# Optimization experiments

Measured on AMD Instinct MI355X. Metric: run time of the kernel, lower is better.

## Reference

```python
import jax, jax.numpy as jnp
import numpy as np
from jax import lax

D = 2048; H = 32; N = 64; S = 2048
LW = 64; LA = 64; LG = 128; LV = 32


def _ln(z, w, b, eps):
    m = jnp.mean(z, axis=-1, keepdims=True)
    v = jnp.var(z, axis=-1, keepdims=True)
    return (z - m) * lax.rsqrt(v + eps) * w + b


def setup_inputs():
    ks = iter(jax.random.split(jax.random.key(0), 40))
    nrm = lambda shape, s=1.0: jax.random.normal(next(ks), shape, dtype=jnp.float32) * s
    return {
        "x": nrm((1, S, D)),
        "state1": nrm((D,)),
        "state2": nrm((H, N, N), 0.1),
        "v_first": nrm((S, H, N)),
        "ln1_w": jnp.ones((D,), jnp.float32),
        "ln1_b": jnp.zeros((D,), jnp.float32),
        "x_r": nrm((D,), 0.1), "x_w": nrm((D,), 0.1), "x_k": nrm((D,), 0.1),
        "x_v": nrm((D,), 0.1), "x_a": nrm((D,), 0.1), "x_g": nrm((D,), 0.1),
        "Wr": nrm((D, D), 0.02), "Wk": nrm((D, D), 0.02),
        "Wv": nrm((D, D), 0.02), "Wo": nrm((D, D), 0.02),
        "w1": nrm((D, LW), 0.02), "w2": nrm((LW, D), 0.05), "w0": nrm((D,), 0.1),
        "a1": nrm((D, LA), 0.02), "a2": nrm((LA, D), 0.05), "a0": nrm((D,), 0.1),
        "g1": nrm((D, LG), 0.02), "g2": nrm((LG, D), 0.05),
        "v1": nrm((D, LV), 0.02), "v2": nrm((LV, D), 0.05), "v0": nrm((D,), 0.1),
        "k_k": nrm((H, N), 0.5), "k_a": nrm((H, N), 0.5), "r_k": nrm((H, N), 0.5),
        "ln_x_w": jnp.ones((D,), jnp.float32),
        "ln_x_b": jnp.zeros((D,), jnp.float32),
    }


def _forward(x, state1, state2, v_first, ln1_w, ln1_b, x_r, x_w, x_k, x_v, x_a, x_g,
             Wr, Wk, Wv, Wo, w1, w2, w0, a1, a2, a0, g1, g2, v1, v2, v0,
             k_k, k_a, r_k, ln_x_w, ln_x_b):
    last_x = x
    xn = _ln(x, ln1_w, ln1_b, 1e-5)                      # (1,S,D)
    state1_out = xn[:, -1:]
    past = jnp.concatenate([state1.reshape(1, 1, D), xn[:, :-1]], axis=1)
    sx = past - xn                                        # token-shift delta
    xr = xn + sx * x_r; xw = xn + sx * x_w; xk = xn + sx * x_k
    xv = xn + sx * x_v; xa = xn + sx * x_a; xg = xn + sx * x_g
    r = (xr @ Wr.T).reshape(S, H, N)
    k = (xk @ Wk.T).reshape(S, H, N)
    v = (xv @ Wv.T).reshape(S, H, N)
    gate = jax.nn.sigmoid(xg @ g1) @ g2                   # (1,S,D)
    a = jax.nn.sigmoid((xa @ a1) @ a2 + a0).reshape(S, H, N)
    td = jnp.tanh(xw @ w1) @ w2 + w0
    w_dec = jnp.exp(-0.606531 * jax.nn.sigmoid(td)).reshape(S, H, N)
    kk = k * k_k
    kk = kk / jnp.maximum(jnp.linalg.norm(kk, axis=-1, keepdims=True), 1e-12)
    k = k * (1.0 + (a - 1.0) * k_a)
    # layer_id != 0: residual value mixing with v_first
    v = v + (v_first - v) * jax.nn.sigmoid(((xv @ v1) @ v2 + v0).reshape(S, H, N))
    b = kk * a
    a_neg = -kk

    def step(s, inp):
        # s: (H,N,N) state; each input (H,N)
        r_t, w_t, k_t, v_t, a_t, b_t = inp
        sa = jnp.einsum('hij,hj->hi', s, a_t)
        s = s * w_t[:, None, :] + sa[:, :, None] * b_t[:, None, :] + v_t[:, :, None] * k_t[:, None, :]
        return s, jnp.einsum('hij,hj->hi', s, r_t)

    state2_out, y = lax.scan(step, state2, (r, w_dec, k, v, a_neg, b))  # y: (S,H,N)
    o = _ln(y, 1.0, 0.0, 0.00064).reshape(1, S, D)       # ln_x (default affine)
    o = o * ln_x_w + ln_x_b
    rkv = (jnp.sum(r * k * r_k, axis=-1, keepdims=True) * v).reshape(1, S, D)
    o = (o + rkv) * gate
    o = o @ Wo.T
    return last_x + o, state1_out, state2_out


def reference(x, state1, state2, v_first, ln1_w, ln1_b, x_r, x_w, x_k, x_v, x_a, x_g,
              Wr, Wk, Wv, Wo, w1, w2, w0, a1, a2, a0, g1, g2, v1, v2, v0,
              k_k, k_a, r_k, ln_x_w, ln_x_b):
    return _forward(x, state1, state2, v_first, ln1_w, ln1_b, x_r, x_w, x_k, x_v, x_a, x_g,
                    Wr, Wk, Wv, Wo, w1, w2, w0, a1, a2, a0, g1, g2, v1, v2, v0,
                    k_k, k_a, r_k, ln_x_w, ln_x_b)
```

## Files before the change

kernel.cpp:

```cpp
#include <hip/hip_runtime.h>
#include <math.h>

#define kD 2048
#define kH 32
#define kN 64
#define kS 2048

typedef unsigned short ushort_t;
typedef unsigned int uint32;

__device__ __forceinline__ ushort_t f2bf(float f) {
  uint32 u = __float_as_uint(f);
  u += 0x7fffu + ((u >> 16) & 1u);
  return (ushort_t)(u >> 16);
}
__device__ __forceinline__ float bf2f(ushort_t u) {
  return __uint_as_float(((uint32)u) << 16);
}
__device__ __forceinline__ float sigm(float x) { return 1.f / (1.f + __expf(-x)); }

__global__ __launch_bounds__(256) void ln1_kernel(
    const float* __restrict__ x, const float* __restrict__ w, const float* __restrict__ b,
    ushort_t* __restrict__ xnbf, ushort_t* __restrict__ xprevbf,
    const float* __restrict__ state1, float* __restrict__ state1_out)
{
  int t = blockIdx.x;
  const float* row = x + (size_t)t * kD;
  float s = 0.f, s2 = 0.f;
  for (int d = threadIdx.x; d < kD; d += 256) {
    float v = row[d]; s += v; s2 += v * v;
  }
  #pragma unroll
  for (int o = 32; o > 0; o >>= 1) { s += __shfl_down(s, o); s2 += __shfl_down(s2, o); }
  __shared__ float ls[4], ls2[4];
  int wid = threadIdx.x >> 6;
  if ((threadIdx.x & 63) == 0) { ls[wid] = s; ls2[wid] = s2; }
  __syncthreads();
  s = ls[0] + ls[1] + ls[2] + ls[3];
  s2 = ls2[0] + ls2[1] + ls2[2] + ls2[3];
  float mean = s * (1.f / kD);
  float var = s2 * (1.f / kD) - mean * mean;
  float rstd = rsqrtf(var + 1e-5f);
  for (int d = threadIdx.x; d < kD; d += 256) {
    float v = (row[d] - mean) * rstd * w[d] + b[d];
    ushort_t bf = f2bf(v);
    xnbf[(size_t)t * kD + d] = bf;
    if (t < kS - 1) xprevbf[(size_t)(t + 1) * kD + d] = bf;
    else state1_out[d] = v;
    if (t == 0) xprevbf[d] = f2bf(state1[d]);
  }
}

__global__ __launch_bounds__(256) void mix3_cvt(
    const ushort_t* __restrict__ xnbf, const ushort_t* __restrict__ xprevbf,
    const float* __restrict__ cr, const float* __restrict__ ck, const float* __restrict__ cv,
    ushort_t* __restrict__ Ar, ushort_t* __restrict__ Ak, ushort_t* __restrict__ Av)
{
  int t = blockIdx.x;
  size_t base = (size_t)t * kD;
  for (int d = threadIdx.x; d < kD; d += 256) {
    float c = bf2f(xnbf[base + d]);
    float dx = bf2f(xprevbf[base + d]) - c;
    Ar[base + d] = f2bf(c + dx * cr[d]);
    Ak[base + d] = f2bf(c + dx * ck[d]);
    Av[base + d] = f2bf(c + dx * cv[d]);
  }
}

struct CvtArgs { const float* src[3]; ushort_t* dst[3]; };
__global__ __launch_bounds__(256) void cvt_bf16_b(CvtArgs args)
{
  const float* in = args.src[blockIdx.y];
  ushort_t* out = args.dst[blockIdx.y];
  int idx = blockIdx.x * 256 + threadIdx.x;
  float4 v = ((const float4*)in)[idx];
  ushort_t o[4] = { f2bf(v.x), f2bf(v.y), f2bf(v.z), f2bf(v.w) };
  ((uint2*)out)[idx] = *(const uint2*)o;
}

typedef __bf16 bf16x8 __attribute__((ext_vector_type(8)));
typedef float f32x4 __attribute__((ext_vector_type(4)));

struct GemmArgs {
  const ushort_t* A[3];
  const ushort_t* B[3];
  float* C[3];
  const float* resid[3];
};

__global__ __launch_bounds__(256) void gemm_bf16_b(GemmArgs args)
{
  int z = blockIdx.z;
  const ushort_t* __restrict__ A = args.A[z];
  const ushort_t* __restrict__ B = args.B[z];
  float* __restrict__ C = args.C[z];
  const float* __restrict__ resid = args.resid[z];

  __shared__ __align__(16) ushort_t As[128 * 64];
  __shared__ __align__(16) ushort_t Bs[128 * 64];
  int tid = threadIdx.x;
  int w = tid >> 6, lane = tid & 63;
  int row0 = blockIdx.y * 128, col0 = blockIdx.x * 128;
  int wrow = (w >> 1) * 64, wcol = (w & 1) * 64;
  int quad = lane >> 4, r16 = lane & 15;
  f32x4 acc[4][4] = {};

  int lrow = lane >> 3;
  int lsw  = (lane & 7) ^ lrow;

  for (int k0 = 0; k0 < kD; k0 += 64) {
    #pragma unroll
    for (int n = 0; n < 4; n++) {
      int rr = w * 32 + n * 8 + lrow;
      int cc = k0 + lsw * 8;
      const ushort_t* ga = A + (size_t)(row0 + rr) * kD + cc;
      const ushort_t* gb = B + (size_t)(col0 + rr) * kD + cc;
      __builtin_amdgcn_global_load_lds(
          (const __attribute__((address_space(1))) uint32*)ga,
          (__attribute__((address_space(3))) uint32*)&As[(w * 32 + n * 8) * 64], 16, 0, 0);
      __builtin_amdgcn_global_load_lds(
          (const __attribute__((address_space(1))) uint32*)gb,
          (__attribute__((address_space(3))) uint32*)&Bs[(w * 32 + n * 8) * 64], 16, 0, 0);
    }
    __syncthreads();
    #pragma unroll
    for (int kk = 0; kk < 64; kk += 32) {
      bf16x8 af[4], bfr[4];
      #pragma unroll
      for (int i = 0; i < 4; i++) {
        int row = wrow + i * 16 + r16;
        int chunk = ((kk >> 3) + quad) ^ (r16 & 7);
        af[i] = *(const bf16x8*)&As[row * 64 + chunk * 8];
      }
      #pragma unroll
      for (int j = 0; j < 4; j++) {
        int row = wcol + j * 16 + r16;
        int chunk = ((kk >> 3) + quad) ^ (r16 & 7);
        bfr[j] = *(const bf16x8*)&Bs[row * 64 + chunk * 8];
      }
      #pragma unroll
      for (int i = 0; i < 4; i++)
        #pragma unroll
        for (int j = 0; j < 4; j++)
          acc[i][j] = __builtin_amdgcn_mfma_f32_16x16x32_bf16(af[i], bfr[j], acc[i][j], 0, 0, 0);
    }
    __syncthreads();
  }
  #pragma unroll
  for (int i = 0; i < 4; i++) {
    #pragma unroll
    for (int j = 0; j < 4; j++) {
      int col = col0 + wcol + j * 16 + r16;
      #pragma unroll
      for (int reg = 0; reg < 4; reg++) {
        int row = row0 + wrow + i * 16 + quad * 4 + reg;
        float v = acc[i][j][reg];
        if (resid) v += resid[(size_t)row * kD + col];
        C[(size_t)row * kD + col] = v;
      }
    }
  }
}

struct PrepW1Args { const float* w1[4]; const float* c[4]; ushort_t* B1; };
__global__ __launch_bounds__(256) void prep_w1(PrepW1Args a)
{
  __shared__ float tile[64][17];
  int k0 = blockIdx.x * 64;
  int col0 = blockIdx.y * 16;
  int z, lc0, L;
  if (col0 < 128)      { z = 0; lc0 = col0;       L = 128; }
  else if (col0 < 192) { z = 1; lc0 = col0 - 128; L = 64; }
  else if (col0 < 256) { z = 2; lc0 = col0 - 192; L = 64; }
  else if (col0 < 288) { z = 3; lc0 = col0 - 256; L = 32; }
  else z = -1;
  int tid = threadIdx.x;
  if (z >= 0) {
    const float* W = a.w1[z];
    const float* C = a.c[z];
    int cc = tid & 15, kk = tid >> 4;
    #pragma unroll
    for (int i = 0; i < 4; i++) {
      int k = k0 + kk + i * 16;
      int ksrc = k & (kD - 1);
      float cv = C[ksrc];
      float sc = (k < kD) ? (1.f - cv) : cv;
      tile[kk + i * 16][cc] = W[(size_t)ksrc * L + lc0 + cc] * sc;
    }
  }
  __syncthreads();
  int kk2 = tid & 63, cc2 = tid >> 6;
  #pragma unroll
  for (int i = 0; i < 4; i++) {
    int col = col0 + cc2 * 4 + i;
    float v = (z >= 0) ? tile[kk2][cc2 * 4 + i] : 0.f;
    a.B1[(size_t)col * 4096 + k0 + kk2] = f2bf(v);
  }
}

struct PrepW2Args { const float* w2[4]; ushort_t* B2[4]; int L[4]; };
__global__ __launch_bounds__(256) void prep_w2(PrepW2Args a)
{
  __shared__ float tile[64][17];
  int z = blockIdx.z;
  int L = a.L[z];
  int l0 = blockIdx.y * 16;
  if (l0 >= L) return;
  int j0 = blockIdx.x * 64;
  int tid = threadIdx.x;
  const float* W = a.w2[z];
  ushort_t* out = a.B2[z];
  int jj = tid & 63;
  #pragma unroll
  for (int i = 0; i < 4; i++) {
    int ll = (tid >> 6) * 4 + i;
    tile[jj][ll] = W[(size_t)(l0 + ll) * kD + j0 + jj];
  }
  __syncthreads();
  int ll2 = tid & 15;
  #pragma unroll
  for (int i = 0; i < 4; i++) {
    int jj2 = (tid >> 4) + i * 16;
    out[(size_t)(j0 + jj2) * L + l0 + ll2] = f2bf(tile[jj2][ll2]);
  }
}

__global__ __launch_bounds__(256) void gemm1_kernel(
    const ushort_t* __restrict__ xnbf, const ushort_t* __restrict__ xprevbf,
    const ushort_t* __restrict__ B1, ushort_t* __restrict__ H)
{
  __shared__ __align__(16) ushort_t As[128 * 64];
  __shared__ __align__(16) ushort_t Bs[64 * 64];
  int tid = threadIdx.x;
  int w = tid >> 6, lane = tid & 63;
  int col0 = blockIdx.x * 64, row0 = blockIdx.y * 128;
  int quad = lane >> 4, r16 = lane & 15;
  f32x4 acc[2][4] = {};
  int lrow = lane >> 3;
  int lsw = (lane & 7) ^ lrow;

  for (int k0 = 0; k0 < 4096; k0 += 64) {
    const ushort_t* Abase = (k0 < kD) ? (xnbf + k0) : (xprevbf + (k0 - kD));
    #pragma unroll
    for (int n = 0; n < 4; n++) {
      int rr = w * 32 + n * 8 + lrow;
      const ushort_t* ga = Abase + (size_t)(row0 + rr) * kD + lsw * 8;
      __builtin_amdgcn_global_load_lds(
          (const __attribute__((address_space(1))) uint32*)ga,
          (__attribute__((address_space(3))) uint32*)&As[(w * 32 + n * 8) * 64], 16, 0, 0);
    }
    #pragma unroll
    for (int n = 0; n < 2; n++) {
      int rr = w * 16 + n * 8 + lrow;
      const ushort_t* gb = B1 + (size_t)(col0 + rr) * 4096 + k0 + lsw * 8;
      __builtin_amdgcn_global_load_lds(
          (const __attribute__((address_space(1))) uint32*)gb,
          (__attribute__((address_space(3))) uint32*)&Bs[(w * 16 + n * 8) * 64], 16, 0, 0);
    }
    __syncthreads();
    #pragma unroll
    for (int kk = 0; kk < 64; kk += 32) {
      bf16x8 af[2], bfr[4];
      #pragma unroll
      for (int i = 0; i < 2; i++) {
        int row = w * 32 + i * 16 + r16;
        int chunk = ((kk >> 3) + quad) ^ (r16 & 7);
        af[i] = *(const bf16x8*)&As[row * 64 + chunk * 8];
      }
      #pragma unroll
      for (int j = 0; j < 4; j++) {
        int row = j * 16 + r16;
        int chunk = ((kk >> 3) + quad) ^ (r16 & 7);
        bfr[j] = *(const bf16x8*)&Bs[row * 64 + chunk * 8];
      }
      #pragma unroll
      for (int i = 0; i < 2; i++)
        #pragma unroll
        for (int j = 0; j < 4; j++)
          acc[i][j] = __builtin_amdgcn_mfma_f32_16x16x32_bf16(af[i], bfr[j], acc[i][j], 0, 0, 0);
    }
    __syncthreads();
  }
  #pragma unroll
  for (int i = 0; i < 2; i++) {
    #pragma unroll
    for (int j = 0; j < 4; j++) {
      int col = col0 + j * 16 + r16;
      #pragma unroll
      for (int reg = 0; reg < 4; reg++) {
        int row = row0 + w * 32 + i * 16 + quad * 4 + reg;
        float v = acc[i][j][reg];
        if (col < 128) v = sigm(v);
        else if (col >= 192 && col < 256) v = tanhf(v);
        H[(size_t)row * 320 + col] = f2bf(v);
      }
    }
  }
}

struct Gemm2Args {
  const ushort_t* H;
  const ushort_t* B2[4];
  int Aofs[4];
  int L[4];
  const float* bias[4];
  float* out[4];
  const float* vfirst;
};
__global__ __launch_bounds__(256) void gemm2_kernel(Gemm2Args a)
{
  int z = blockIdx.z;
  int L = a.L[z];
  int nch = L >> 3;
  int rs = __builtin_ctz(nch);
  int mask = (nch >= 8) ? 7 : (nch - 1);
  __shared__ __align__(16) ushort_t As[128 * 128];
  __shared__ __align__(16) ushort_t Bs[128 * 128];
  int tid = threadIdx.x;
  int w = tid >> 6, lane = tid & 63;
  int row0 = blockIdx.y * 128, col0 = blockIdx.x * 128;
  int wrow = (w >> 1) * 64, wcol = (w & 1) * 64;
  int quad = lane >> 4, r16 = lane & 15;
  const ushort_t* A = a.H + a.Aofs[z];
  const ushort_t* B = a.B2[z];

  int nld = (128 * nch) >> 8;
  for (int i = 0; i < nld; i++) {
    int c = i * 256 + w * 64 + lane;
    int row = c >> rs;
    int ch = c & (nch - 1);
    int gch = ch ^ (row & mask);
    __builtin_amdgcn_global_load_lds(
        (const __attribute__((address_space(1))) uint32*)(A + (size_t)(row0 + row) * 320 + gch * 8),
        (__attribute__((address_space(3))) uint32*)&As[(i * 256 + w * 64) * 8], 16, 0, 0);
    __builtin_amdgcn_global_load_lds(
        (const __attribute__((address_space(1))) uint32*)(B + (size_t)(col0 + row) * L + gch * 8),
        (__attribute__((address_space(3))) uint32*)&Bs[(i * 256 + w * 64) * 8], 16, 0, 0);
  }
  __syncthreads();

  f32x4 acc[4][4] = {};
  int ksteps = L >> 5;
  for (int ks = 0; ks < ksteps; ks++) {
    bf16x8 af[4], bfr[4];
    #pragma unroll
    for (int i = 0; i < 4; i++) {
      int row = wrow + i * 16 + r16;
      int slot = ((ks << 2) + quad) ^ (r16 & mask);
      af[i] = *(const bf16x8*)&As[row * L + slot * 8];
    }
    #pragma unroll
    for (int j = 0; j < 4; j++) {
      int row = wcol + j * 16 + r16;
      int slot = ((ks << 2) + quad) ^ (r16 & mask);
      bfr[j] = *(const bf16x8*)&Bs[row * L + slot * 8];
    }
    #pragma unroll
    for (int i = 0; i < 4; i++)
      #pragma unroll
      for (int j = 0; j < 4; j++)
        acc[i][j] = __builtin_amdgcn_mfma_f32_16x16x32_bf16(af[i], bfr[j], acc[i][j], 0, 0, 0);
  }

  const float* bias = a.bias[z];
  float* C = a.out[z];
  #pragma unroll
  for (int i = 0; i < 4; i++) {
    #pragma unroll
    for (int j = 0; j < 4; j++) {
      int col = col0 + wcol + j * 16 + r16;
      #pragma unroll
      for (int reg = 0; reg < 4; reg++) {
        int row = row0 + wrow + i * 16 + quad * 4 + reg;
        float s = acc[i][j][reg];
        size_t idx = (size_t)row * kD + col;
        if (z == 0) {
          C[idx] = s;
        } else if (z == 1) {
          C[idx] = sigm(s + bias[col]);
        } else if (z == 2) {
          C[idx] = __expf(-0.606531f * sigm(s + bias[col]));
        } else {
          float vv = C[idx];
          C[idx] = vv + (a.vfirst[idx] - vv) * sigm(s + bias[col]);
        }
      }
    }
  }
}

__global__ __launch_bounds__(256) void post_kernel(
    float* __restrict__ kArr, float* __restrict__ kkArr, float* __restrict__ bArr,
    const float* __restrict__ aArr, float* __restrict__ rArr, const float* __restrict__ wArr,
    const float* __restrict__ k_k, const float* __restrict__ k_a, const float* __restrict__ r_k,
    float* __restrict__ c12, float* __restrict__ c3)
{
  int gid = blockIdx.x * 4 + (threadIdx.x >> 6);
  int lane = threadIdx.x & 63;
  int h = gid & (kH - 1);
  int d = h * kN + lane;
  size_t off = (size_t)gid * kN + lane;
  float kv = kArr[off];
  float kkv = kv * k_k[d];
  float ss = kkv * kkv;
  #pragma unroll
  for (int o = 32; o > 0; o >>= 1) ss += __shfl_xor(ss, o);
  float scale = 1.f / fmaxf(sqrtf(ss), 1e-12f);
  float kkf = kkv * scale;
  kkArr[off] = -kkf;
  float av = aArr[off];
  float bv = kkf * av;
  bArr[off] = bv;
  float knew = kv * (1.f + (av - 1.f) * k_a[d]);
  kArr[off] = knew;
  float rv = rArr[off];
  float wv = wArr[off];
  rArr[off] = wv * rv;
  float p1 = bv * rv;
  float p2 = knew * rv;
  float p3 = rv * knew * r_k[d];
  #pragma unroll
  for (int o = 32; o > 0; o >>= 1) {
    p1 += __shfl_xor(p1, o); p2 += __shfl_xor(p2, o); p3 += __shfl_xor(p3, o);
  }
  if (lane == 0) {
    c12[(size_t)gid * 2]     = p1;
    c12[(size_t)gid * 2 + 1] = p2;
    c3[gid] = p3;
  }
}

#define SLOT_F 344
#define NSLOT 24

__device__ __forceinline__ void row_allsum2(float& x, float& y) {
  int t;
  t = __builtin_amdgcn_update_dpp(0, __float_as_int(x), 0x121, 0xF, 0xF, true);
  x += __int_as_float(t);
  t = __builtin_amdgcn_update_dpp(0, __float_as_int(y), 0x121, 0xF, 0xF, true);
  y += __int_as_float(t);
  t = __builtin_amdgcn_update_dpp(0, __float_as_int(x), 0x122, 0xF, 0xF, true);
  x += __int_as_float(t);
  t = __builtin_amdgcn_update_dpp(0, __float_as_int(y), 0x122, 0xF, 0xF, true);
  y += __int_as_float(t);
  t = __builtin_amdgcn_update_dpp(0, __float_as_int(x), 0x124, 0xF, 0xF, true);
  x += __int_as_float(t);
  t = __builtin_amdgcn_update_dpp(0, __float_as_int(y), 0x124, 0xF, 0xF, true);
  y += __int_as_float(t);
  t = __builtin_amdgcn_update_dpp(0, __float_as_int(x), 0x128, 0xF, 0xF, true);
  x += __int_as_float(t);
  t = __builtin_amdgcn_update_dpp(0, __float_as_int(y), 0x128, 0xF, 0xF, true);
  y += __int_as_float(t);
}

__global__ __launch_bounds__(320) void scan_kernel(
    const float* __restrict__ s0_in, const float* __restrict__ wA, const float* __restrict__ wrA,
    const float* __restrict__ kA, const float* __restrict__ vA, const float* __restrict__ kkA,
    const float* __restrict__ bA, const float* __restrict__ c12,
    float* __restrict__ y, float* __restrict__ s_out)
{
  __shared__ __align__(16) float ring[NSLOT * SLOT_F];
  int blk = blockIdx.x;
  int h = blk >> 2;
  int i0 = (blk & 3) << 4;
  int wid = threadIdx.x >> 6;
  int lane = threadIdx.x & 63;
  int hv = h * kN;

  if (wid == 0) {
    const float* src0 = wA + hv;
    const float* src1 = wrA + hv;
    const float* src2 = kA + hv;
    const float* src3 = kkA + hv;
    const float* src4 = bA + hv;
    const float* vsrc = vA + hv + i0;
    const float* csrc = c12 + (size_t)h * 2;
    int slot = 0;
    #define ISSUE(t)                                                                     \
      {                                                                                  \
        float* sb = &ring[slot * SLOT_F];                                                \
        size_t go = (size_t)(t) * kD + lane;                                             \
        __builtin_amdgcn_global_load_lds(                                                \
            (const __attribute__((address_space(1))) uint32*)(src0 + go),                \
            (__attribute__((address_space(3))) uint32*)(sb + 0), 4, 0, 0);               \
        __builtin_amdgcn_global_load_lds(                                                \
            (const __attribute__((address_space(1))) uint32*)(src1 + go),                \
            (__attribute__((address_space(3))) uint32*)(sb + 64), 4, 0, 0);              \
        __builtin_amdgcn_global_load_lds(                                                \
            (const __attribute__((address_space(1))) uint32*)(src2 + go),                \
            (__attribute__((address_space(3))) uint32*)(sb + 128), 4, 0, 0);             \
        __builtin_amdgcn_global_load_lds(                                                \
            (const __attribute__((address_space(1))) uint32*)(src3 + go),                \
            (__attribute__((address_space(3))) uint32*)(sb + 192), 4, 0, 0);             \
        __builtin_amdgcn_global_load_lds(                                                \
            (const __attribute__((address_space(1))) uint32*)(src4 + go),                \
            (__attribute__((address_space(3))) uint32*)(sb + 256), 4, 0, 0);             \
        if (lane < 16)                                                                   \
          __builtin_amdgcn_global_load_lds(                                              \
              (const __attribute__((address_space(1))) uint32*)(vsrc + (size_t)(t) * kD + lane), \
              (__attribute__((address_space(3))) uint32*)(sb + 320), 4, 0, 0);           \
        if (lane < 2)                                                                    \
          __builtin_amdgcn_global_load_lds(                                              \
              (const __attribute__((address_space(1))) uint32*)(csrc + (size_t)(t) * (kH * 2) + lane), \
              (__attribute__((address_space(3))) uint32*)(sb + 336), 4, 0, 0);           \
        slot++; if (slot == NSLOT) slot = 0;                                             \
      }
    for (int t = 0; t < 16; t++) ISSUE(t);
    __syncthreads();
    for (int ph = 0; ph < kS / 8; ph++) {
      int t0 = ph * 8 + 16;
      if (t0 < kS) {
        for (int s = 0; s < 8; s++) ISSUE(t0 + s);
      }
      __syncthreads();
    }
    #undef ISSUE
  } else {
    int col16 = lane & 15;
    int row = lane >> 4;
    int vidx = (wid - 1) * 4 + row;
    int i = i0 + vidx;
    int co = col16 * 4;
    size_t srow = ((size_t)(hv + i)) * kN + co;
    float4 sS = *(const float4*)(s0_in + srow);
    float* py = y + (size_t)(hv + i);

    __syncthreads();

    float4 Aw4, Awr4, Ak4, Akk4, Ab4; float Av1, Ac1, Ac2;
    float4 Bw4, Bwr4, Bk4, Bkk4, Bb4; float Bv1, Bc1, Bc2;

    #define LOADSLOT(sl, W, WR, K, KK, B, V, C1, C2)             \
      {                                                          \
        const float* sb = &ring[(sl) * SLOT_F];                  \
        W  = *(const float4*)(sb + co);                          \
        WR = *(const float4*)(sb + 64 + co);                     \
        K  = *(const float4*)(sb + 128 + co);                    \
        KK = *(const float4*)(sb + 192 + co);                    \
        B  = *(const float4*)(sb + 256 + co);                    \
        V  = sb[320 + vidx];                                     \
        C1 = sb[336];                                            \
        C2 = sb[337];                                            \
      }
    #define STEP(W, WR, K, KK, B, V, C1, C2)                                  \
      {                                                                       \
        float sa = sS.x * KK.x + sS.y * KK.y + sS.z * KK.z + sS.w * KK.w;     \
        float u  = sS.x * WR.x + sS.y * WR.y + sS.z * WR.z + sS.w * WR.w;     \
        row_allsum2(sa, u);                                                   \
        sS.x = fmaf(sS.x, W.x, fmaf(sa, B.x, V * K.x));                       \
        sS.y = fmaf(sS.y, W.y, fmaf(sa, B.y, V * K.y));                       \
        sS.z = fmaf(sS.z, W.z, fmaf(sa, B.z, V * K.z));                       \
        sS.w = fmaf(sS.w, W.w, fmaf(sa, B.w, V * K.w));                       \
        float yv = fmaf(sa, C1, fmaf(V, C2, u));                              \
        if (col16 == 0) *py = yv;                                             \
        py += kD;                                                             \
      }

    LOADSLOT(0, Aw4, Awr4, Ak4, Akk4, Ab4, Av1, Ac1, Ac2);
    int slot = 1;
    for (int ph = 0; ph < kS / 8; ph++) {
      #pragma unroll
      for (int s = 0; s < 8; s += 2) {
        LOADSLOT(slot, Bw4, Bwr4, Bk4, Bkk4, Bb4, Bv1, Bc1, Bc2);
        slot++; if (slot == NSLOT) slot = 0;
        STEP(Aw4, Awr4, Ak4, Akk4, Ab4, Av1, Ac1, Ac2);
        LOADSLOT(slot, Aw4, Awr4, Ak4, Akk4, Ab4, Av1, Ac1, Ac2);
        slot++; if (slot == NSLOT) slot = 0;
        STEP(Bw4, Bwr4, Bk4, Bkk4, Bb4, Bv1, Bc1, Bc2);
      }
      __syncthreads();
    }
    #undef LOADSLOT
    #undef STEP
    *(float4*)(s_out + srow) = sS;
  }
}

__global__ __launch_bounds__(256) void out_kernel(
    const float* __restrict__ y, const float* __restrict__ vA, const float* __restrict__ c3,
    const float* __restrict__ lnw, const float* __restrict__ lnb,
    const float* __restrict__ gate, ushort_t* __restrict__ Ay)
{
  int gid = blockIdx.x * 4 + (threadIdx.x >> 6);
  int lane = threadIdx.x & 63;
  int h = gid & (kH - 1);
  size_t off = (size_t)gid * kN + lane;
  float yv = y[off];
  float s = yv, s2 = yv * yv;
  #pragma unroll
  for (int o = 32; o > 0; o >>= 1) { s += __shfl_xor(s, o); s2 += __shfl_xor(s2, o); }
  float mean = s * (1.f / kN);
  float var = s2 * (1.f / kN) - mean * mean;
  float o1 = (yv - mean) * rsqrtf(var + 0.00064f);
  int d = h * kN + lane;
  float ov = o1 * lnw[d] + lnb[d];
  float rkv = c3[gid] * vA[off];
  Ay[off] = f2bf((ov + rkv) * gate[off]);
}

extern "C" void kernel_launch(void* const* d_in, const int* in_sizes, int n_in,
                              void* d_out, int out_size, void* d_ws, size_t ws_size,
                              hipStream_t stream)
{
  const float* x      = (const float*)d_in[0];
  const float* state1 = (const float*)d_in[1];
  const float* state2 = (const float*)d_in[2];
  const float* vfirst = (const float*)d_in[3];
  const float* ln1w   = (const float*)d_in[4];
  const float* ln1b   = (const float*)d_in[5];
  const float* xr_c   = (const float*)d_in[6];
  const float* xw_c   = (const float*)d_in[7];
  const float* xk_c   = (const float*)d_in[8];
  const float* xv_c   = (const float*)d_in[9];
  const float* xa_c   = (const float*)d_in[10];
  const float* xg_c   = (const float*)d_in[11];
  const float* Wr     = (const float*)d_in[12];
  const float* Wk     = (const float*)d_in[13];
  const float* Wv     = (const float*)d_in[14];
  const float* Wo     = (const float*)d_in[15];
  const float* w1     = (const float*)d_in[16];
  const float* w2     = (const float*)d_in[17];
  const float* w0     = (const float*)d_in[18];
  const float* a1     = (const float*)d_in[19];
  const float* a2     = (const float*)d_in[20];
  const float* a0     = (const float*)d_in[21];
  const float* g1     = (const float*)d_in[22];
  const float* g2     = (const float*)d_in[23];
  const float* v1     = (const float*)d_in[24];
  const float* v2     = (const float*)d_in[25];
  const float* v0     = (const float*)d_in[26];
  const float* k_k    = (const float*)d_in[27];
  const float* k_a    = (const float*)d_in[28];
  const float* r_k    = (const float*)d_in[29];
  const float* lnxw   = (const float*)d_in[30];
  const float* lnxb   = (const float*)d_in[31];

  float* out0  = (float*)d_out;
  float* s1out = out0 + (size_t)kS * kD;
  float* s2out = s1out + kD;

  size_t SD = (size_t)kS * kD;
  float* ws  = (float*)d_ws;
  float* xnB = ws;
  float* rB  = ws + SD;
  float* kB  = ws + 2 * SD;
  float* vB  = ws + 3 * SD;
  float* wB  = ws + 4 * SD;
  float* aB  = ws + 5 * SD;
  float* kkB = ws + 6 * SD;
  float* bB  = ws + 7 * SD;
  float* gB  = ws + 8 * SD;
  float* yB  = ws + 9 * SD;

  ushort_t* xnbf    = (ushort_t*)xnB;
  ushort_t* xprevbf = (ushort_t*)xnB + SD;
  ushort_t* ArB = (ushort_t*)kkB;
  ushort_t* AkB = (ushort_t*)kkB + SD;
  ushort_t* AvB = (ushort_t*)bB;
  ushort_t* B1  = (ushort_t*)bB + SD;
  ushort_t* Hbuf = B1 + (size_t)320 * 4096;
  ushort_t* B2g  = Hbuf + (size_t)2048 * 320;
  ushort_t* B2a  = B2g + (size_t)2048 * 128;
  ushort_t* B2w  = B2a + (size_t)2048 * 64;
  ushort_t* B2v  = B2w + (size_t)2048 * 64;
  ushort_t* WrB = (ushort_t*)yB;
  ushort_t* WkB = (ushort_t*)yB + SD;
  ushort_t* WvB = (ushort_t*)gB;
  ushort_t* AyB = (ushort_t*)aB;
  ushort_t* WoB = (ushort_t*)rB;
  float* c12B = xnB;
  float* c3B  = xnB + (size_t)kS * kH * 2;

  ln1_kernel<<<kS, 256, 0, stream>>>(x, ln1w, ln1b, xnbf, xprevbf, state1, s1out);
  mix3_cvt<<<kS, 256, 0, stream>>>(xnbf, xprevbf, xr_c, xk_c, xv_c, ArB, AkB, AvB);

  const int CVT_BLKS = (int)(SD / 4 / 256);
  {
    CvtArgs ca;
    ca.src[0] = Wr; ca.src[1] = Wk; ca.src[2] = Wv;
    ca.dst[0] = WrB; ca.dst[1] = WkB; ca.dst[2] = WvB;
    cvt_bf16_b<<<dim3(CVT_BLKS, 3), 256, 0, stream>>>(ca);
  }
  {
    PrepW1Args pa;
    pa.w1[0] = g1; pa.w1[1] = a1; pa.w1[2] = w1; pa.w1[3] = v1;
    pa.c[0] = xg_c; pa.c[1] = xa_c; pa.c[2] = xw_c; pa.c[3] = xv_c;
    pa.B1 = B1;
    prep_w1<<<dim3(64, 20), 256, 0, stream>>>(pa);
  }
  {
    PrepW2Args pa;
    pa.w2[0] = g2; pa.w2[1] = a2; pa.w2[2] = w2; pa.w2[3] = v2;
    pa.B2[0] = B2g; pa.B2[1] = B2a; pa.B2[2] = B2w; pa.B2[3] = B2v;
    pa.L[0] = 128; pa.L[1] = 64; pa.L[2] = 64; pa.L[3] = 32;
    prep_w2<<<dim3(32, 8, 4), 256, 0, stream>>>(pa);
  }
  {
    GemmArgs ga;
    ga.A[0] = ArB; ga.A[1] = AkB; ga.A[2] = AvB;
    ga.B[0] = WrB; ga.B[1] = WkB; ga.B[2] = WvB;
    ga.C[0] = rB;  ga.C[1] = kB;  ga.C[2] = vB;
    ga.resid[0] = nullptr; ga.resid[1] = nullptr; ga.resid[2] = nullptr;
    gemm_bf16_b<<<dim3(16, 16, 3), 256, 0, stream>>>(ga);
  }

  gemm1_kernel<<<dim3(5, 16), 256, 0, stream>>>(xnbf, xprevbf, B1, Hbuf);
  {
    Gemm2Args ga;
    ga.H = Hbuf;
    ga.B2[0] = B2g; ga.B2[1] = B2a; ga.B2[2] = B2w; ga.B2[3] = B2v;
    ga.Aofs[0] = 0; ga.Aofs[1] = 128; ga.Aofs[2] = 192; ga.Aofs[3] = 256;
    ga.L[0] = 128; ga.L[1] = 64; ga.L[2] = 64; ga.L[3] = 32;
    ga.bias[0] = nullptr; ga.bias[1] = a0; ga.bias[2] = w0; ga.bias[3] = v0;
    ga.out[0] = gB; ga.out[1] = aB; ga.out[2] = wB; ga.out[3] = vB;
    ga.vfirst = vfirst;
    gemm2_kernel<<<dim3(16, 16, 4), 256, 0, stream>>>(ga);
  }

  post_kernel<<<kS * kH / 4, 256, 0, stream>>>(kB, kkB, bB, aB, rB, wB,
                                               k_k, k_a, r_k, c12B, c3B);

  scan_kernel<<<kH * 4, 320, 0, stream>>>(state2, wB, rB, kB, vB, kkB, bB, c12B, yB, s2out);

  out_kernel<<<kS * kH / 4, 256, 0, stream>>>(yB, vB, c3B, lnxw, lnxb, gB, AyB);

  {
    CvtArgs ca;
    ca.src[0] = Wo; ca.src[1] = Wo; ca.src[2] = Wo;
    ca.dst[0] = WoB; ca.dst[1] = WoB; ca.dst[2] = WoB;
    cvt_bf16_b<<<dim3(CVT_BLKS, 1), 256, 0, stream>>>(ca);
  }
  {
    GemmArgs ga;
    ga.A[0] = AyB; ga.A[1] = AyB; ga.A[2] = AyB;
    ga.B[0] = WoB; ga.B[1] = WoB; ga.B[2] = WoB;
    ga.C[0] = out0; ga.C[1] = out0; ga.C[2] = out0;
    ga.resid[0] = x; ga.resid[1] = x; ga.resid[2] = x;
    gemm_bf16_b<<<dim3(16, 16, 1), 256, 0, stream>>>(ga);
  }
}
```

Measured before the change: 795.8 us.

## Use 16-byte global_load_lds in scan producer and widen ring phases

The scan kernel's producer wave now issues two 16-byte-per-lane global-to-LDS loads per timestep instead of seven 4-byte loads. Lanes are assigned to the w/wr/k/kk rows, the b row, the v slice and the padded c12 pair. c12 is padded to a stride of 4 floats so it stays 16-byte aligned. The ring grows to 32 slots with 16-step phases, which halves barrier frequency, and blocks are remapped so neighbouring blocks cover different heads. The aim is to cut per-step load-issue overhead and barrier syncs on the serial recurrence, at the cost of more LDS use.

```diff
diff --git a/kernel.cpp b/kernel.cpp
--- a/kernel.cpp
+++ b/kernel.cpp
@@ -424,14 +424,15 @@
     p1 += __shfl_xor(p1, o); p2 += __shfl_xor(p2, o); p3 += __shfl_xor(p3, o);
   }
   if (lane == 0) {
-    c12[(size_t)gid * 2]     = p1;
-    c12[(size_t)gid * 2 + 1] = p2;
+    c12[(size_t)gid * 4]     = p1;
+    c12[(size_t)gid * 4 + 1] = p2;
     c3[gid] = p3;
   }
 }
 
 #define SLOT_F 344
-#define NSLOT 24
+#define NSLOT 32
+#define PHASE 16
 
 __device__ __forceinline__ void row_allsum2(float& x, float& y) {
   int t;
@@ -461,56 +462,40 @@
 {
   __shared__ __align__(16) float ring[NSLOT * SLOT_F];
   int blk = blockIdx.x;
-  int h = blk >> 2;
-  int i0 = (blk & 3) << 4;
+  int h = blk & 31;
+  int i0 = (blk >> 5) << 4;
   int wid = threadIdx.x >> 6;
   int lane = threadIdx.x & 63;
   int hv = h * kN;
 
   if (wid == 0) {
-    const float* src0 = wA + hv;
-    const float* src1 = wrA + hv;
-    const float* src2 = kA + hv;
-    const float* src3 = kkA + hv;
-    const float* src4 = bA + hv;
-    const float* vsrc = vA + hv + i0;
-    const float* csrc = c12 + (size_t)h * 2;
-    int slot = 0;
-    #define ISSUE(t)                                                                     \
-      {                                                                                  \
-        float* sb = &ring[slot * SLOT_F];                                                \
-        size_t go = (size_t)(t) * kD + lane;                                             \
-        __builtin_amdgcn_global_load_lds(                                                \
-            (const __attribute__((address_space(1))) uint32*)(src0 + go),                \
-            (__attribute__((address_space(3))) uint32*)(sb + 0), 4, 0, 0);               \
-        __builtin_amdgcn_global_load_lds(                                                \
-            (const __attribute__((address_space(1))) uint32*)(src1 + go),                \
-            (__attribute__((address_space(3))) uint32*)(sb + 64), 4, 0, 0);              \
-        __builtin_amdgcn_global_load_lds(                                                \
-            (const __attribute__((address_space(1))) uint32*)(src2 + go),                \
-            (__attribute__((address_space(3))) uint32*)(sb + 128), 4, 0, 0);             \
-        __builtin_amdgcn_global_load_lds(                                                \
-            (const __attribute__((address_space(1))) uint32*)(src3 + go),                \
-            (__attribute__((address_space(3))) uint32*)(sb + 192), 4, 0, 0);             \
-        __builtin_amdgcn_global_load_lds(                                                \
-            (const __attribute__((address_space(1))) uint32*)(src4 + go),                \
-            (__attribute__((address_space(3))) uint32*)(sb + 256), 4, 0, 0);             \
-        if (lane < 16)                                                                   \
-          __builtin_amdgcn_global_load_lds(                                              \
-              (const __attribute__((address_space(1))) uint32*)(vsrc + (size_t)(t) * kD + lane), \
-              (__attribute__((address_space(3))) uint32*)(sb + 320), 4, 0, 0);           \
-        if (lane < 2)                                                                    \
-          __builtin_amdgcn_global_load_lds(                                              \
-              (const __attribute__((address_space(1))) uint32*)(csrc + (size_t)(t) * (kH * 2) + lane), \
-              (__attribute__((address_space(3))) uint32*)(sb + 336), 4, 0, 0);           \
-        slot++; if (slot == NSLOT) slot = 0;                                             \
-      }
-    for (int t = 0; t < 16; t++) ISSUE(t);
+    int sel = lane >> 4;
+    const float* b1 = (sel == 0) ? wA : (sel == 1) ? wrA : (sel == 2) ? kA : kkA;
+    b1 += hv + (lane & 15) * 4;
+    const float* b2;
+    size_t st2;
+    if (lane < 16)      { b2 = bA + hv + lane * 4;             st2 = kD; }
+    else if (lane < 20) { b2 = vA + hv + i0 + (lane - 16) * 4; st2 = kD; }
+    else                { b2 = c12 + (size_t)h * 4;            st2 = kH * 4; }
+    bool m2 = (lane < 21);
+
+    #define ISSUE(t)                                                                       \
+      {                                                                                    \
+        float* sb = &ring[((t) & (NSLOT - 1)) * SLOT_F];                                   \
+        __builtin_amdgcn_global_load_lds(                                                  \
+            (const __attribute__((address_space(1))) uint32*)(b1 + (size_t)(t) * kD),      \
+            (__attribute__((address_space(3))) uint32*)sb, 16, 0, 0);                      \
+        if (m2)                                                                            \
+          __builtin_amdgcn_global_load_lds(                                                \
+              (const __attribute__((address_space(1))) uint32*)(b2 + (size_t)(t) * st2),   \
+              (__attribute__((address_space(3))) uint32*)(sb + 256), 16, 0, 0);            \
+      }
+    for (int t = 0; t < PHASE; t++) ISSUE(t);
     __syncthreads();
-    for (int ph = 0; ph < kS / 8; ph++) {
-      int t0 = ph * 8 + 16;
+    for (int ph = 0; ph < kS / PHASE; ph++) {
+      int t0 = ph * PHASE + PHASE;
       if (t0 < kS) {
-        for (int s = 0; s < 8; s++) ISSUE(t0 + s);
+        for (int t = t0; t < t0 + PHASE; t++) ISSUE(t);
       }
       __syncthreads();
     }
@@ -556,16 +541,15 @@
         py += kD;                                                             \
       }
 
-    LOADSLOT(0, Aw4, Awr4, Ak4, Akk4, Ab4, Av1, Ac1, Ac2);
-    int slot = 1;
-    for (int ph = 0; ph < kS / 8; ph++) {
-      #pragma unroll
-      for (int s = 0; s < 8; s += 2) {
-        LOADSLOT(slot, Bw4, Bwr4, Bk4, Bkk4, Bb4, Bv1, Bc1, Bc2);
-        slot++; if (slot == NSLOT) slot = 0;
+    for (int ph = 0; ph < kS / PHASE; ph++) {
+      int t0 = ph * PHASE;
+      LOADSLOT(t0 & (NSLOT - 1), Aw4, Awr4, Ak4, Akk4, Ab4, Av1, Ac1, Ac2);
+      #pragma unroll
+      for (int s = 0; s < PHASE; s += 2) {
+        LOADSLOT((t0 + s + 1) & (NSLOT - 1), Bw4, Bwr4, Bk4, Bkk4, Bb4, Bv1, Bc1, Bc2);
         STEP(Aw4, Awr4, Ak4, Akk4, Ab4, Av1, Ac1, Ac2);
-        LOADSLOT(slot, Aw4, Awr4, Ak4, Akk4, Ab4, Av1, Ac1, Ac2);
-        slot++; if (slot == NSLOT) slot = 0;
+        if (s + 2 < PHASE)
+          LOADSLOT((t0 + s + 2) & (NSLOT - 1), Aw4, Awr4, Ak4, Akk4, Ab4, Av1, Ac1, Ac2);
         STEP(Bw4, Bwr4, Bk4, Bkk4, Bb4, Bv1, Bc1, Bc2);
       }
       __syncthreads();
@@ -669,7 +653,7 @@
   ushort_t* AyB = (ushort_t*)aB;
   ushort_t* WoB = (ushort_t*)rB;
   float* c12B = xnB;
-  float* c3B  = xnB + (size_t)kS * kH * 2;
+  float* c3B  = xnB + (size_t)kS * kH * 4;
 
   ln1_kernel<<<kS, 256, 0, stream>>>(x, ln1w, ln1b, xnbf, xprevbf, state1, s1out);
   mix3_cvt<<<kS, 256, 0, stream>>>(xnbf, xprevbf, xr_c, xk_c, xv_c, ArB, AkB, AvB);
```

Result: faster. 736.5 us (-7.4%).
